# Optimization experiments

Measured on AMD Instinct MI355X. Metric: run time of the kernel, lower is better.

Reference implementation:

```python
import jax, jax.numpy as jnp
import numpy as np

VOCAB = 32000; EMB = 1024; HID = 1024
NLAYERS = 2; NBLOCKS = 2; BATCH = 8; SEQ = 256
LN_EPS = 1e-5


def _xavier(key, shape):
    fan_out, fan_in = shape[-2], shape[-1]
    bound = float(np.sqrt(6.0 / (fan_in + fan_out)))
    return jax.random.uniform(key, shape, jnp.float32, -bound, bound)


def setup_inputs() -> dict:
    key = jax.random.key(0)
    k = jax.random.split(key, 8)
    return {
        "input_seq": jax.random.randint(k[0], (BATCH, SEQ), 0, VOCAB),
        "embedding": _xavier(k[1], (VOCAB, EMB)),
        "w_ih": _xavier(k[2], (NBLOCKS, NLAYERS, 4 * HID, HID)),
        "w_hh": _xavier(k[3], (NBLOCKS, NLAYERS, 4 * HID, HID)),
        "bias": jnp.zeros((NBLOCKS, NLAYERS, 4 * HID), jnp.float32),
        "ln_gamma": jnp.ones((NBLOCKS, HID), jnp.float32),
        "ln_beta": jnp.zeros((NBLOCKS, HID), jnp.float32),
        "out_w": _xavier(k[4], (VOCAB, HID)),
        "out_b": jnp.zeros((VOCAB,), jnp.float32),
    }


def _slstm_block(x_seq, w_ih, w_hh, b, ln_g, ln_b):
    """One xLSTMBlock: stacked sLSTM layers (exp gating) + GELU + residual + LayerNorm.
    x_seq: [B,S,H]; w_ih/w_hh: [L,4H,H]; b: [L,4H]."""
    B, S, H = x_seq.shape
    L = w_ih.shape[0]

    def step(carry, x_t):
        hs, cs = carry                  # each [L,B,H]
        inp = x_t                       # [B,H]
        new_hs, new_cs = [], []
        for l in range(L):              # fixed small layer count -> ok to unroll
            gates = inp @ w_ih[l].T + hs[l] @ w_hh[l].T + b[l]   # [B,4H]
            i, f, g, o = jnp.split(gates, 4, axis=-1)
            c = jnp.exp(f) * cs[l] + jnp.exp(i) * jnp.tanh(g)    # exponential gating
            h = jax.nn.sigmoid(o) * jnp.tanh(c)
            new_hs.append(h)
            new_cs.append(c)
            inp = h
        return (jnp.stack(new_hs), jnp.stack(new_cs)), inp

    init = (jnp.zeros((L, B, H), x_seq.dtype), jnp.zeros((L, B, H), x_seq.dtype))
    _, out = jax.lax.scan(step, init, jnp.swapaxes(x_seq, 0, 1))  # out: [S,B,H]
    out = jnp.swapaxes(out, 0, 1)                                 # [B,S,H]
    out = jax.nn.gelu(out, approximate=False) + x_seq             # activation + residual
    mu = out.mean(-1, keepdims=True)
    var = out.var(-1, keepdims=True)
    return (out - mu) * jax.lax.rsqrt(var + LN_EPS) * ln_g + ln_b


def reference(input_seq, embedding, w_ih, w_hh, bias, ln_gamma, ln_beta, out_w, out_b):
    x = embedding[input_seq]                                      # [B,S,E]
    for blk in range(NBLOCKS):
        x = _slstm_block(x, w_ih[blk], w_hh[blk], bias[blk], ln_gamma[blk], ln_beta[blk])
    return x @ out_w.T + out_b                                    # logits [B,S,V]
```

## Files before the change

kernel.cpp:

```cpp
#include <hip/hip_runtime.h>
#include <stdint.h>
#include <math.h>

#define SEQ   256
#define BATCH 8
#define HID   1024
#define VOCAB 32000

typedef __attribute__((ext_vector_type(8))) short s16x8;
typedef __attribute__((ext_vector_type(4))) float f32x4;

__device__ __forceinline__ unsigned short f2bf(float f) {
    union { float f; uint32_t u; } v; v.f = f;
    uint32_t r = v.u + 0x7fffu + ((v.u >> 16) & 1u);
    return (unsigned short)(r >> 16);
}
__device__ __forceinline__ float bf2f(unsigned short h) {
    union { float f; uint32_t u; } v; v.u = ((uint32_t)h) << 16;
    return v.f;
}

__global__ __launch_bounds__(256)
void k_embed(const int* __restrict__ idx, const float* __restrict__ emb,
             float* __restrict__ x) {
    const int row = blockIdx.x;
    const int id  = idx[row];
    const f32x4 v = *(const f32x4*)(emb + (size_t)id*HID + threadIdx.x*4);
    *(f32x4*)(x + (size_t)row*HID + threadIdx.x*4) = v;
}

__global__ __launch_bounds__(256)
void k_cvt(const float* __restrict__ in, unsigned short* __restrict__ hi,
           unsigned short* __restrict__ lo, int n) {
    for (int i = blockIdx.x*blockDim.x + threadIdx.x; i < n; i += gridDim.x*blockDim.x) {
        float f = in[i];
        unsigned short h = f2bf(f);
        hi[i] = h;
        lo[i] = f2bf(f - bf2f(h));
    }
}

__global__ __launch_bounds__(256)
void k_gemm_f64(const float* __restrict__ A, const float* __restrict__ B,
                double* __restrict__ C, int M, int N, int K) {
    __shared__ float As[64][33];
    __shared__ float Bs[64][33];
    const int nbn = N >> 6;
    const int bm = blockIdx.x / nbn, bn = blockIdx.x % nbn;
    const int tid = threadIdx.x;
    const int tr = tid >> 4, tc = tid & 15;
    const int lr = tid >> 2, lc = (tid & 3) << 3;
    double acc[4][4];
    #pragma unroll
    for (int r = 0; r < 4; ++r)
        #pragma unroll
        for (int c = 0; c < 4; ++c) acc[r][c] = 0.0;
    const float* Ag = A + (size_t)(bm*64 + lr)*K + lc;
    const float* Bg = B + (size_t)(bn*64 + lr)*K + lc;
    for (int k0 = 0; k0 < K; k0 += 32) {
        f32x4 a0 = *(const f32x4*)(Ag + k0);
        f32x4 a1 = *(const f32x4*)(Ag + k0 + 4);
        f32x4 b0 = *(const f32x4*)(Bg + k0);
        f32x4 b1 = *(const f32x4*)(Bg + k0 + 4);
        __syncthreads();
        #pragma unroll
        for (int e = 0; e < 4; ++e) {
            As[lr][lc + e]     = a0[e];
            As[lr][lc + 4 + e] = a1[e];
            Bs[lr][lc + e]     = b0[e];
            Bs[lr][lc + 4 + e] = b1[e];
        }
        __syncthreads();
        #pragma unroll
        for (int kk = 0; kk < 32; ++kk) {
            double ad[4], bd[4];
            #pragma unroll
            for (int r = 0; r < 4; ++r) ad[r] = (double)As[tr*4 + r][kk];
            #pragma unroll
            for (int c = 0; c < 4; ++c) bd[c] = (double)Bs[tc*4 + c][kk];
            #pragma unroll
            for (int r = 0; r < 4; ++r)
                #pragma unroll
                for (int c = 0; c < 4; ++c)
                    acc[r][c] = fma(ad[r], bd[c], acc[r][c]);
        }
    }
    #pragma unroll
    for (int r = 0; r < 4; ++r) {
        double* Cr = C + (size_t)(bm*64 + tr*4 + r)*N + bn*64 + tc*4;
        #pragma unroll
        for (int c = 0; c < 4; ++c) Cr[c] = acc[r][c];
    }
}

__global__ __launch_bounds__(256)
void k_gemm3(const unsigned short* __restrict__ Ahi,
             const unsigned short* __restrict__ Alo,
             const unsigned short* __restrict__ Bhi,
             const unsigned short* __restrict__ Blo,
             float* __restrict__ C,
             const float* __restrict__ bias,
             int M, int N, int K) {
    __shared__ unsigned short Ash[128][32];
    __shared__ unsigned short Asl[128][32];
    __shared__ unsigned short Bsh[128][32];
    __shared__ unsigned short Bsl[128][32];
    const int nbn = N >> 7;
    const int bm = blockIdx.x / nbn, bn = blockIdx.x % nbn;
    const int tid = threadIdx.x;
    const int lane = tid & 63, wave = tid >> 6;
    const int wr = wave >> 1, wc = wave & 1;
    const int lrow = tid >> 2, lcol = (tid & 3) << 3;
    const size_t aoff = (size_t)(bm*128 + lrow)*K + lcol;
    const size_t boff = (size_t)(bn*128 + lrow)*K + lcol;
    const int frow = lane & 15, fk = (lane >> 4) << 3;

    f32x4 acc[4][4];
    #pragma unroll
    for (int i = 0; i < 4; ++i)
        #pragma unroll
        for (int j = 0; j < 4; ++j)
            #pragma unroll
            for (int e = 0; e < 4; ++e) acc[i][j][e] = 0.f;

    for (int k0 = 0; k0 < K; k0 += 32) {
        uint4 ah0 = *(const uint4*)(Ahi + aoff + k0);
        uint4 ah1 = *(const uint4*)(Ahi + aoff + (size_t)64*K + k0);
        uint4 al0 = *(const uint4*)(Alo + aoff + k0);
        uint4 al1 = *(const uint4*)(Alo + aoff + (size_t)64*K + k0);
        uint4 bh0 = *(const uint4*)(Bhi + boff + k0);
        uint4 bh1 = *(const uint4*)(Bhi + boff + (size_t)64*K + k0);
        uint4 bl0 = *(const uint4*)(Blo + boff + k0);
        uint4 bl1 = *(const uint4*)(Blo + boff + (size_t)64*K + k0);
        __syncthreads();
        *(uint4*)&Ash[lrow][lcol]      = ah0;
        *(uint4*)&Ash[lrow + 64][lcol] = ah1;
        *(uint4*)&Asl[lrow][lcol]      = al0;
        *(uint4*)&Asl[lrow + 64][lcol] = al1;
        *(uint4*)&Bsh[lrow][lcol]      = bh0;
        *(uint4*)&Bsh[lrow + 64][lcol] = bh1;
        *(uint4*)&Bsl[lrow][lcol]      = bl0;
        *(uint4*)&Bsl[lrow + 64][lcol] = bl1;
        __syncthreads();
        s16x8 ah[4], al[4], bh[4], bl[4];
        #pragma unroll
        for (int mi = 0; mi < 4; ++mi) {
            ah[mi] = *(const s16x8*)&Ash[wr*64 + mi*16 + frow][fk];
            al[mi] = *(const s16x8*)&Asl[wr*64 + mi*16 + frow][fk];
        }
        #pragma unroll
        for (int ni = 0; ni < 4; ++ni) {
            bh[ni] = *(const s16x8*)&Bsh[wc*64 + ni*16 + frow][fk];
            bl[ni] = *(const s16x8*)&Bsl[wc*64 + ni*16 + frow][fk];
        }
        #pragma unroll
        for (int mi = 0; mi < 4; ++mi)
            #pragma unroll
            for (int ni = 0; ni < 4; ++ni) {
                acc[mi][ni] = __builtin_amdgcn_mfma_f32_16x16x32_bf16(ah[mi], bh[ni], acc[mi][ni], 0, 0, 0);
                acc[mi][ni] = __builtin_amdgcn_mfma_f32_16x16x32_bf16(ah[mi], bl[ni], acc[mi][ni], 0, 0, 0);
                acc[mi][ni] = __builtin_amdgcn_mfma_f32_16x16x32_bf16(al[mi], bh[ni], acc[mi][ni], 0, 0, 0);
            }
    }

    #pragma unroll
    for (int mi = 0; mi < 4; ++mi) {
        const int row0 = bm*128 + wr*64 + mi*16 + ((lane >> 4) << 2);
        #pragma unroll
        for (int ni = 0; ni < 4; ++ni) {
            const int col = bn*128 + wc*64 + ni*16 + (lane & 15);
            const float bv = bias ? bias[col] : 0.f;
            #pragma unroll
            for (int r = 0; r < 4; ++r) {
                const size_t ix = (size_t)(row0 + r)*N + col;
                C[ix] = acc[mi][ni][r] + bv;
            }
        }
    }
}

__global__ __launch_bounds__(256)
void k_scan(const float* __restrict__ whh0,
            const float* __restrict__ wih1,
            const float* __restrict__ whh1,
            const float* __restrict__ bias0,
            const float* __restrict__ bias1,
            const double* __restrict__ G0,
            float* h0, double* c0, float* h1, double* c1,
            float* __restrict__ y,
            int k) {
    const int wgid = blockIdx.x;
    const int wave = threadIdx.x >> 6;
    const int lane = threadIdx.x & 63;
    const int HB = BATCH * HID;

    if (wgid < 256) {
        if (k >= SEQ) return;
        const int t = k;
        const int u = wgid*4 + wave;
        const float* hp = h0 + ((k + 1) & 1) * HB;
        double acc[4][8];
        #pragma unroll
        for (int g = 0; g < 4; ++g)
            #pragma unroll
            for (int b = 0; b < 8; ++b) acc[g][b] = 0.0;
        #pragma unroll
        for (int jj = 0; jj < 4; ++jj) {
            const int kb = 4*lane + 256*jj;
            double hd[8][4];
            #pragma unroll
            for (int b = 0; b < 8; ++b) {
                const f32x4 hv = *(const f32x4*)(hp + b*HID + kb);
                #pragma unroll
                for (int e = 0; e < 4; ++e) hd[b][e] = (double)hv[e];
            }
            #pragma unroll
            for (int g = 0; g < 4; ++g) {
                const f32x4 wv = *(const f32x4*)(whh0 + (size_t)(g*HID + u)*HID + kb);
                double wd[4];
                #pragma unroll
                for (int e = 0; e < 4; ++e) wd[e] = (double)wv[e];
                #pragma unroll
                for (int b = 0; b < 8; ++b)
                    #pragma unroll
                    for (int e = 0; e < 4; ++e)
                        acc[g][b] = fma(wd[e], hd[b][e], acc[g][b]);
            }
        }
        #pragma unroll
        for (int g = 0; g < 4; ++g)
            #pragma unroll
            for (int b = 0; b < 8; ++b) {
                double v = acc[g][b];
                #pragma unroll
                for (int off = 32; off > 0; off >>= 1) v += __shfl_xor(v, off, 64);
                acc[g][b] = v;
            }
        if (lane < 8) {
            const int b = lane;
            const double* g0r = G0 + (size_t)(b*SEQ + t)*4096;
            const double gi = acc[0][b] + g0r[u]         + (double)bias0[u];
            const double gf = acc[1][b] + g0r[HID + u]   + (double)bias0[HID + u];
            const double gg = acc[2][b] + g0r[2*HID + u] + (double)bias0[2*HID + u];
            const double go = acc[3][b] + g0r[3*HID + u] + (double)bias0[3*HID + u];
            const double cc = exp(gf)*c0[b*HID + u] + exp(gi)*tanh(gg);
            const double hh = tanh(cc) / (1.0 + exp(-go));
            c0[b*HID + u] = cc;
            h0[(k & 1)*HB + b*HID + u] = (float)hh;
        }
    } else {
        if (k < 1) return;
        const int t = k - 1;
        const int u = (wgid - 256)*4 + wave;
        const float* hin = h0 + ((k + 1) & 1) * HB;
        const float* hpp = h1 + (k & 1) * HB;
        double acc[4][8];
        #pragma unroll
        for (int g = 0; g < 4; ++g)
            #pragma unroll
            for (int b = 0; b < 8; ++b) acc[g][b] = 0.0;
        #pragma unroll
        for (int jj = 0; jj < 4; ++jj) {
            const int kb = 4*lane + 256*jj;
            double hd[8][4];
            #pragma unroll
            for (int b = 0; b < 8; ++b) {
                const f32x4 hv = *(const f32x4*)(hin + b*HID + kb);
                #pragma unroll
                for (int e = 0; e < 4; ++e) hd[b][e] = (double)hv[e];
            }
            #pragma unroll
            for (int g = 0; g < 4; ++g) {
                const f32x4 wv = *(const f32x4*)(wih1 + (size_t)(g*HID + u)*HID + kb);
                double wd[4];
                #pragma unroll
                for (int e = 0; e < 4; ++e) wd[e] = (double)wv[e];
                #pragma unroll
                for (int b = 0; b < 8; ++b)
                    #pragma unroll
                    for (int e = 0; e < 4; ++e)
                        acc[g][b] = fma(wd[e], hd[b][e], acc[g][b]);
            }
            #pragma unroll
            for (int b = 0; b < 8; ++b) {
                const f32x4 hv = *(const f32x4*)(hpp + b*HID + kb);
                #pragma unroll
                for (int e = 0; e < 4; ++e) hd[b][e] = (double)hv[e];
            }
            #pragma unroll
            for (int g = 0; g < 4; ++g) {
                const f32x4 wv = *(const f32x4*)(whh1 + (size_t)(g*HID + u)*HID + kb);
                double wd[4];
                #pragma unroll
                for (int e = 0; e < 4; ++e) wd[e] = (double)wv[e];
                #pragma unroll
                for (int b = 0; b < 8; ++b)
                    #pragma unroll
                    for (int e = 0; e < 4; ++e)
                        acc[g][b] = fma(wd[e], hd[b][e], acc[g][b]);
            }
        }
        #pragma unroll
        for (int g = 0; g < 4; ++g)
            #pragma unroll
            for (int b = 0; b < 8; ++b) {
                double v = acc[g][b];
                #pragma unroll
                for (int off = 32; off > 0; off >>= 1) v += __shfl_xor(v, off, 64);
                acc[g][b] = v;
            }
        if (lane < 8) {
            const int b = lane;
            const double gi = acc[0][b] + (double)bias1[u];
            const double gf = acc[1][b] + (double)bias1[HID + u];
            const double gg = acc[2][b] + (double)bias1[2*HID + u];
            const double go = acc[3][b] + (double)bias1[3*HID + u];
            const double cc = exp(gf)*c1[b*HID + u] + exp(gi)*tanh(gg);
            const double hh = tanh(cc) / (1.0 + exp(-go));
            c1[b*HID + u] = cc;
            h1[((k + 1) & 1)*HB + b*HID + u] = (float)hh;
            y[(size_t)(b*SEQ + t)*HID + u] = (float)hh;
        }
    }
}

__global__ __launch_bounds__(256)
void k_post(const float* __restrict__ y, const float* __restrict__ xin,
            const float* __restrict__ gamma, const float* __restrict__ beta,
            float* __restrict__ xout) {
    const int row = blockIdx.x;
    const int tid = threadIdx.x;
    const f32x4 v  = *(const f32x4*)(y   + (size_t)row*HID + tid*4);
    const f32x4 xr = *(const f32x4*)(xin + (size_t)row*HID + tid*4);
    double o[4]; double s = 0.0, q = 0.0;
    #pragma unroll
    for (int e = 0; e < 4; ++e) {
        const double t  = (double)v[e];
        const double ge = 0.5 * t * (1.0 + erf(t * 0.7071067811865476));
        const double u  = ge + (double)xr[e];
        o[e] = u; s += u; q += u*u;
    }
    #pragma unroll
    for (int off = 32; off > 0; off >>= 1) {
        s += __shfl_xor(s, off, 64);
        q += __shfl_xor(q, off, 64);
    }
    __shared__ double rs[4], rq[4];
    const int wv = tid >> 6, lane = tid & 63;
    if (lane == 0) { rs[wv] = s; rq[wv] = q; }
    __syncthreads();
    s = rs[0] + rs[1] + rs[2] + rs[3];
    q = rq[0] + rq[1] + rq[2] + rq[3];
    const double mu   = s * (1.0/HID);
    const double var  = q * (1.0/HID) - mu*mu;
    const double rstd = 1.0 / sqrt(var + 1e-5);
    f32x4 ov;
    #pragma unroll
    for (int e = 0; e < 4; ++e) {
        const int col = tid*4 + e;
        ov[e] = (float)((o[e] - mu)*rstd*(double)gamma[col] + (double)beta[col]);
    }
    *(f32x4*)(xout + (size_t)row*HID + tid*4) = ov;
}

extern "C" void kernel_launch(void* const* d_in, const int* in_sizes, int n_in,
                              void* d_out, int out_size, void* d_ws, size_t ws_size,
                              hipStream_t stream) {
    const int*   idx   = (const int*)d_in[0];
    const float* emb   = (const float*)d_in[1];
    const float* w_ih  = (const float*)d_in[2];
    const float* w_hh  = (const float*)d_in[3];
    const float* bias  = (const float*)d_in[4];
    const float* ln_g  = (const float*)d_in[5];
    const float* ln_b  = (const float*)d_in[6];
    const float* out_w = (const float*)d_in[7];
    const float* out_b = (const float*)d_in[8];
    float* logits = (float*)d_out;

    char* ws = (char*)d_ws;
    size_t off = 0;
    auto alloc = [&](size_t bytes) -> char* {
        char* p = ws + off;
        off = (off + bytes + 255) & ~(size_t)255;
        return p;
    };
    const int ROWS = BATCH * SEQ;
    float*          X    = (float*)         alloc((size_t)ROWS*HID*4);
    unsigned short* XHI  = (unsigned short*)alloc((size_t)ROWS*HID*2);
    unsigned short* XLO  = (unsigned short*)alloc((size_t)ROWS*HID*2);
    char*           ST   =                  alloc(262144);
    char*           REG  = alloc((size_t)VOCAB*HID*2*2);
    double*         G0p  = (double*)REG;
    float*          Y    = (float*)(REG + (size_t)ROWS*4096*8);
    unsigned short* OWHI = (unsigned short*)REG;
    unsigned short* OWLO = (unsigned short*)(REG + (size_t)VOCAB*HID*2);

    float*  h0 = (float*)ST;
    float*  h1 = (float*)(ST + 65536);
    double* c0 = (double*)(ST + 131072);
    double* c1 = (double*)(ST + 196608);

    k_embed<<<ROWS, 256, 0, stream>>>(idx, emb, X);

    for (int blk = 0; blk < 2; ++blk) {
        const float* wih_b = w_ih + (size_t)blk*2*4096*HID;
        const float* whh_b = w_hh + (size_t)blk*2*4096*HID;
        const float* b0 = bias + (size_t)blk*2*4096;
        const float* b1 = b0 + 4096;

        k_gemm_f64<<<(ROWS/64)*(4096/64), 256, 0, stream>>>(X, wih_b, G0p,
                                                            ROWS, 4096, HID);

        hipMemsetAsync(ST, 0, 262144, stream);

        const float* whh0 = whh_b;
        const float* wih1 = wih_b + (size_t)4096*HID;
        const float* whh1 = whh_b + (size_t)4096*HID;
        for (int kk = 0; kk <= SEQ; ++kk)
            k_scan<<<512, 256, 0, stream>>>(whh0, wih1, whh1, b0, b1, G0p,
                                            h0, c0, h1, c1, Y, kk);

        k_post<<<ROWS, 256, 0, stream>>>(Y, X, ln_g + blk*HID, ln_b + blk*HID, X);
    }

    k_cvt<<<1024, 256, 0, stream>>>(X, XHI, XLO, ROWS*HID);
    k_cvt<<<4096, 256, 0, stream>>>(out_w, OWHI, OWLO, VOCAB*HID);
    k_gemm3<<<16*250, 256, 0, stream>>>(XHI, XLO, OWHI, OWLO, logits, out_b,
                                        ROWS, VOCAB, HID);
}
```

Before: 15.57 ms.

## Replace per-step scan launches with persistent cooperative kernel holding weights in registers

Replaces the 257 per-timestep k_scan launches with a single cooperative persistent kernel that loops over timesteps and uses grid.sync between them. Each wave loads its slice of the recurrent (and layer-1 input) weights into registers once, so the weights are not re-read from memory every step. If the cooperative launch fails, it falls back to the old per-step launches. The old kernel's FMA loop is also restructured to drop its temporary double arrays. The risks are high register pressure from holding 32 f32x4 weight values per thread with __launch_bounds__(512,2), and the cost of a grid-wide barrier each step.

```diff
diff --git a/kernel.cpp b/kernel.cpp
--- a/kernel.cpp
+++ b/kernel.cpp
@@ -1,11 +1,15 @@
 #include <hip/hip_runtime.h>
+#include <hip/hip_cooperative_groups.h>
 #include <stdint.h>
 #include <math.h>
+
+namespace cg = cooperative_groups;
 
 #define SEQ   256
 #define BATCH 8
 #define HID   1024
 #define VOCAB 32000
+#define HB    (BATCH*HID)
 
 typedef __attribute__((ext_vector_type(8))) short s16x8;
 typedef __attribute__((ext_vector_type(4))) float f32x4;
@@ -179,6 +183,149 @@
     }
 }
 
+__global__ __launch_bounds__(512, 2)
+void k_scan_persist(const float* __restrict__ whh0,
+                    const float* __restrict__ wih1,
+                    const float* __restrict__ whh1,
+                    const float* __restrict__ bias0,
+                    const float* __restrict__ bias1,
+                    const double* __restrict__ G0,
+                    float* h0, double* c0, float* h1, double* c1,
+                    float* __restrict__ y) {
+    cg::grid_group grid = cg::this_grid();
+    const int wg   = blockIdx.x;
+    const int tid  = threadIdx.x;
+    const int wave = tid >> 6, lane = tid & 63;
+    const bool isA = wave < 4;
+    const int u = wg*4 + (wave & 3);
+
+    f32x4 w0[4][4];
+    f32x4 w1[4][4];
+    {
+        const float* m0 = isA ? whh0 : wih1;
+        #pragma unroll
+        for (int g = 0; g < 4; ++g)
+            #pragma unroll
+            for (int jj = 0; jj < 4; ++jj)
+                w0[g][jj] = *(const f32x4*)(m0 + (size_t)(g*HID + u)*HID + 4*lane + 256*jj);
+        if (!isA) {
+            #pragma unroll
+            for (int g = 0; g < 4; ++g)
+                #pragma unroll
+                for (int jj = 0; jj < 4; ++jj)
+                    w1[g][jj] = *(const f32x4*)(whh1 + (size_t)(g*HID + u)*HID + 4*lane + 256*jj);
+        }
+    }
+
+    for (int k = 0; k <= SEQ; ++k) {
+        if (isA) {
+            if (k < SEQ) {
+                const float* hp = h0 + ((k + 1) & 1) * HB;
+                double acc[4][8];
+                #pragma unroll
+                for (int g = 0; g < 4; ++g)
+                    #pragma unroll
+                    for (int b = 0; b < 8; ++b) acc[g][b] = 0.0;
+                #pragma unroll
+                for (int jj = 0; jj < 4; ++jj) {
+                    const int kb = 4*lane + 256*jj;
+                    #pragma unroll
+                    for (int b = 0; b < 8; ++b) {
+                        const f32x4 hv = *(const f32x4*)(hp + b*HID + kb);
+                        #pragma unroll
+                        for (int g = 0; g < 4; ++g) {
+                            acc[g][b] = fma((double)w0[g][jj].x, (double)hv.x, acc[g][b]);
+                            acc[g][b] = fma((double)w0[g][jj].y, (double)hv.y, acc[g][b]);
+                            acc[g][b] = fma((double)w0[g][jj].z, (double)hv.z, acc[g][b]);
+                            acc[g][b] = fma((double)w0[g][jj].w, (double)hv.w, acc[g][b]);
+                        }
+                    }
+                }
+                #pragma unroll
+                for (int g = 0; g < 4; ++g)
+                    #pragma unroll
+                    for (int b = 0; b < 8; ++b) {
+                        double v = acc[g][b];
+                        #pragma unroll
+                        for (int off = 32; off > 0; off >>= 1) v += __shfl_xor(v, off, 64);
+                        acc[g][b] = v;
+                    }
+                if (lane < 8) {
+                    const int b = lane;
+                    const double* g0r = G0 + (size_t)(b*SEQ + k)*4096;
+                    const double gi = acc[0][b] + g0r[u]         + (double)bias0[u];
+                    const double gf = acc[1][b] + g0r[HID + u]   + (double)bias0[HID + u];
+                    const double gg = acc[2][b] + g0r[2*HID + u] + (double)bias0[2*HID + u];
+                    const double go = acc[3][b] + g0r[3*HID + u] + (double)bias0[3*HID + u];
+                    const double cc = exp(gf)*c0[b*HID + u] + exp(gi)*tanh(gg);
+                    const double hh = tanh(cc) / (1.0 + exp(-go));
+                    c0[b*HID + u] = cc;
+                    h0[(k & 1)*HB + b*HID + u] = (float)hh;
+                }
+            }
+        } else {
+            if (k >= 1) {
+                const int t = k - 1;
+                const float* hin = h0 + ((k + 1) & 1) * HB;
+                const float* hpp = h1 + (k & 1) * HB;
+                double acc[4][8];
+                #pragma unroll
+                for (int g = 0; g < 4; ++g)
+                    #pragma unroll
+                    for (int b = 0; b < 8; ++b) acc[g][b] = 0.0;
+                #pragma unroll
+                for (int jj = 0; jj < 4; ++jj) {
+                    const int kb = 4*lane + 256*jj;
+                    #pragma unroll
+                    for (int b = 0; b < 8; ++b) {
+                        const f32x4 hv = *(const f32x4*)(hin + b*HID + kb);
+                        #pragma unroll
+                        for (int g = 0; g < 4; ++g) {
+                            acc[g][b] = fma((double)w0[g][jj].x, (double)hv.x, acc[g][b]);
+                            acc[g][b] = fma((double)w0[g][jj].y, (double)hv.y, acc[g][b]);
+                            acc[g][b] = fma((double)w0[g][jj].z, (double)hv.z, acc[g][b]);
+                            acc[g][b] = fma((double)w0[g][jj].w, (double)hv.w, acc[g][b]);
+                        }
+                    }
+                    #pragma unroll
+                    for (int b = 0; b < 8; ++b) {
+                        const f32x4 hv = *(const f32x4*)(hpp + b*HID + kb);
+                        #pragma unroll
+                        for (int g = 0; g < 4; ++g) {
+                            acc[g][b] = fma((double)w1[g][jj].x, (double)hv.x, acc[g][b]);
+                            acc[g][b] = fma((double)w1[g][jj].y, (double)hv.y, acc[g][b]);
+                            acc[g][b] = fma((double)w1[g][jj].z, (double)hv.z, acc[g][b]);
+                            acc[g][b] = fma((double)w1[g][jj].w, (double)hv.w, acc[g][b]);
+                        }
+                    }
+                }
+                #pragma unroll
+                for (int g = 0; g < 4; ++g)
+                    #pragma unroll
+                    for (int b = 0; b < 8; ++b) {
+                        double v = acc[g][b];
+                        #pragma unroll
+                        for (int off = 32; off > 0; off >>= 1) v += __shfl_xor(v, off, 64);
+                        acc[g][b] = v;
+                    }
+                if (lane < 8) {
+                    const int b = lane;
+                    const double gi = acc[0][b] + (double)bias1[u];
+                    const double gf = acc[1][b] + (double)bias1[HID + u];
+                    const double gg = acc[2][b] + (double)bias1[2*HID + u];
+                    const double go = acc[3][b] + (double)bias1[3*HID + u];
+                    const double cc = exp(gf)*c1[b*HID + u] + exp(gi)*tanh(gg);
+                    const double hh = tanh(cc) / (1.0 + exp(-go));
+                    c1[b*HID + u] = cc;
+                    h1[((k + 1) & 1)*HB + b*HID + u] = (float)hh;
+                    y[(size_t)(b*SEQ + t)*HID + u] = (float)hh;
+                }
+            }
+        }
+        grid.sync();
+    }
+}
+
 __global__ __launch_bounds__(256)
 void k_scan(const float* __restrict__ whh0,
             const float* __restrict__ wih1,
@@ -187,16 +334,13 @@
             const float* __restrict__ bias1,
             const double* __restrict__ G0,
             float* h0, double* c0, float* h1, double* c1,
-            float* __restrict__ y,
-            int k) {
+            float* __restrict__ y, int k) {
     const int wgid = blockIdx.x;
     const int wave = threadIdx.x >> 6;
     const int lane = threadIdx.x & 63;
-    const int HB = BATCH * HID;
 
     if (wgid < 256) {
         if (k >= SEQ) return;
-        const int t = k;
         const int u = wgid*4 + wave;
         const float* hp = h0 + ((k + 1) & 1) * HB;
         double acc[4][8];
@@ -207,24 +351,17 @@
         #pragma unroll
         for (int jj = 0; jj < 4; ++jj) {
             const int kb = 4*lane + 256*jj;
-            double hd[8][4];
             #pragma unroll
             for (int b = 0; b < 8; ++b) {
                 const f32x4 hv = *(const f32x4*)(hp + b*HID + kb);
                 #pragma unroll
-                for (int e = 0; e < 4; ++e) hd[b][e] = (double)hv[e];
-            }
-            #pragma unroll
-            for (int g = 0; g < 4; ++g) {
-                const f32x4 wv = *(const f32x4*)(whh0 + (size_t)(g*HID + u)*HID + kb);
-                double wd[4];
-                #pragma unroll
-                for (int e = 0; e < 4; ++e) wd[e] = (double)wv[e];
-                #pragma unroll
-                for (int b = 0; b < 8; ++b)
-                    #pragma unroll
-                    for (int e = 0; e < 4; ++e)
-                        acc[g][b] = fma(wd[e], hd[b][e], acc[g][b]);
+                for (int g = 0; g < 4; ++g) {
+                    const f32x4 wv = *(const f32x4*)(whh0 + (size_t)(g*HID + u)*HID + kb);
+                    acc[g][b] = fma((double)wv.x, (double)hv.x, acc[g][b]);
+                    acc[g][b] = fma((double)wv.y, (double)hv.y, acc[g][b]);
+                    acc[g][b] = fma((double)wv.z, (double)hv.z, acc[g][b]);
+                    acc[g][b] = fma((double)wv.w, (double)hv.w, acc[g][b]);
+                }
             }
         }
         #pragma unroll
@@ -238,7 +375,7 @@
             }
         if (lane < 8) {
             const int b = lane;
-            const double* g0r = G0 + (size_t)(b*SEQ + t)*4096;
+            const double* g0r = G0 + (size_t)(b*SEQ + k)*4096;
             const double gi = acc[0][b] + g0r[u]         + (double)bias0[u];
             const double gf = acc[1][b] + g0r[HID + u]   + (double)bias0[HID + u];
             const double gg = acc[2][b] + g0r[2*HID + u] + (double)bias0[2*HID + u];
@@ -262,42 +399,29 @@
         #pragma unroll
         for (int jj = 0; jj < 4; ++jj) {
             const int kb = 4*lane + 256*jj;
-            double hd[8][4];
             #pragma unroll
             for (int b = 0; b < 8; ++b) {
                 const f32x4 hv = *(const f32x4*)(hin + b*HID + kb);
                 #pragma unroll
-                for (int e = 0; e < 4; ++e) hd[b][e] = (double)hv[e];
-            }
-            #pragma unroll
-            for (int g = 0; g < 4; ++g) {
-                const f32x4 wv = *(const f32x4*)(wih1 + (size_t)(g*HID + u)*HID + kb);
-                double wd[4];
-                #pragma unroll
-                for (int e = 0; e < 4; ++e) wd[e] = (double)wv[e];
-                #pragma unroll
-                for (int b = 0; b < 8; ++b)
-                    #pragma unroll
-                    for (int e = 0; e < 4; ++e)
-                        acc[g][b] = fma(wd[e], hd[b][e], acc[g][b]);
+                for (int g = 0; g < 4; ++g) {
+                    const f32x4 wv = *(const f32x4*)(wih1 + (size_t)(g*HID + u)*HID + kb);
+                    acc[g][b] = fma((double)wv.x, (double)hv.x, acc[g][b]);
+                    acc[g][b] = fma((double)wv.y, (double)hv.y, acc[g][b]);
+                    acc[g][b] = fma((double)wv.z, (double)hv.z, acc[g][b]);
+                    acc[g][b] = fma((double)wv.w, (double)hv.w, acc[g][b]);
+                }
             }
             #pragma unroll
             for (int b = 0; b < 8; ++b) {
                 const f32x4 hv = *(const f32x4*)(hpp + b*HID + kb);
                 #pragma unroll
-                for (int e = 0; e < 4; ++e) hd[b][e] = (double)hv[e];
-            }
-            #pragma unroll
-            for (int g = 0; g < 4; ++g) {
-                const f32x4 wv = *(const f32x4*)(whh1 + (size_t)(g*HID + u)*HID + kb);
-                double wd[4];
-                #pragma unroll
-                for (int e = 0; e < 4; ++e) wd[e] = (double)wv[e];
-                #pragma unroll
-                for (int b = 0; b < 8; ++b)
-                    #pragma unroll
-                    for (int e = 0; e < 4; ++e)
-                        acc[g][b] = fma(wd[e], hd[b][e], acc[g][b]);
+                for (int g = 0; g < 4; ++g) {
+                    const f32x4 wv = *(const f32x4*)(whh1 + (size_t)(g*HID + u)*HID + kb);
+                    acc[g][b] = fma((double)wv.x, (double)hv.x, acc[g][b]);
+                    acc[g][b] = fma((double)wv.y, (double)hv.y, acc[g][b]);
+                    acc[g][b] = fma((double)wv.z, (double)hv.z, acc[g][b]);
+                    acc[g][b] = fma((double)wv.w, (double)hv.w, acc[g][b]);
+                }
             }
         }
         #pragma unroll
@@ -416,9 +540,17 @@
         const float* whh0 = whh_b;
         const float* wih1 = wih_b + (size_t)4096*HID;
         const float* whh1 = whh_b + (size_t)4096*HID;
-        for (int kk = 0; kk <= SEQ; ++kk)
-            k_scan<<<512, 256, 0, stream>>>(whh0, wih1, whh1, b0, b1, G0p,
-                                            h0, c0, h1, c1, Y, kk);
+        void* ka[] = {(void*)&whh0, (void*)&wih1, (void*)&whh1,
+                      (void*)&b0, (void*)&b1, (void*)&G0p,
+                      (void*)&h0, (void*)&c0, (void*)&h1, (void*)&c1,
+                      (void*)&Y};
+        hipError_t cerr = hipLaunchCooperativeKernel((const void*)k_scan_persist,
+                                                     dim3(256), dim3(512), ka, 0, stream);
+        if (cerr != hipSuccess) {
+            for (int kk = 0; kk <= SEQ; ++kk)
+                k_scan<<<512, 256, 0, stream>>>(whh0, wih1, whh1, b0, b1, G0p,
+                                                h0, c0, h1, c1, Y, kk);
+        }
 
         k_post<<<ROWS, 256, 0, stream>>>(Y, X, ln_g + blk*HID, ln_b + blk*HID, X);
     }
```

Measured after the change: 33.95 ms. +118.1%, slower.
